# Kernel optimization log

Measured on AMD Instinct MI355X. Metric: run time of the kernel, lower is better.

The kernel has to match this reference:

```python
import jax, jax.numpy as jnp
import numpy as np

EMA_A = 0.4      # exponential moving average decay used in Hash_ExpMovAverage
WIN = 9          # window_size
LN_EPS = 1e-3    # keras LayerNormalization default epsilon


def setup_inputs() -> dict:
    key = jax.random.key(0)
    ks = jax.random.split(key, 8)
    B, N, D, H = 8, 4096, 256, 8
    w = lambda k, shape: jax.random.normal(k, shape, jnp.float32) * 0.05
    return {
        "x": jax.random.normal(ks[0], (B, N, D), jnp.float32),
        "head_kernel": w(ks[1], (D, H, D)),
        "head_bias": w(ks[2], (H, D)),
        "down_kernel": w(ks[3], (H, D, D)),
        "down_bias": w(ks[4], (D,)),
        "value_kernel": w(ks[5], (D, D)),
        "value_bias": w(ks[6], (D,)),
        "ln_gamma": jnp.ones((D,), jnp.float32),
        "ln_beta": jnp.zeros((D,), jnp.float32),
    }


def reference(x, head_kernel, head_bias, down_kernel, down_bias,
              value_kernel, value_bias, ln_gamma, ln_beta):
    B, N, D = x.shape
    half = (WIN - 1) // 2

    # Up_Projection: [B,N,D] -> [B,N,H,D], relu
    q = jax.nn.relu(jnp.einsum('bnd,dhe->bnhe', x, head_kernel) + head_bias)

    # ---- Neighborhoods_Arrangement ----
    # Neighborhood_SimHash: sign codes from relu activations, summed over heads
    codes = 2.0 * jnp.minimum(jnp.ceil(q), 1.0) - 1.0        # [B,N,H,D]
    lsh = jnp.sum(codes, axis=-2)                            # [B,N,D]
    # Hash_ExpMovAverage: sort descending along D, add positional encoding, EMA dot
    pos = jnp.argsort(-lsh, axis=-1)                         # descending order
    lsh_sorted = jnp.take_along_axis(lsh, pos, axis=-1)
    pf = pos.astype(jnp.float32)
    freq = 10.0 ** (-(pf / jnp.float32(D)))                  # 1 / 10**powers
    pe = jnp.sin(freq) * (pf % 2) + jnp.cos(freq) * (1.0 - pf % 2)
    vals = lsh_sorted + pe / EMA_A
    c = EMA_A * (1.0 - EMA_A) ** jnp.arange(D, dtype=jnp.float32)
    simv = jnp.einsum('bnd,d->bn', vals, c)                  # [B,N]
    order = jnp.argsort(simv, axis=-1)                       # ascending
    q = jnp.take_along_axis(q, order[:, :, None, None], axis=1)  # reorder tokens

    # Down_Projection: [B,N,H,D] -> [B,N,D], relu
    q = jax.nn.relu(jnp.einsum('bnhd,hde->bne', q, down_kernel) + down_bias)

    # (matches tile-first / extract_patches / tile-last concat in the original)
    starts = jnp.clip(jnp.arange(N) - half, 0, N - WIN)      # [N]
    widx = starts[:, None] + jnp.arange(WIN)[None, :]
    keyw = q[:, widx]

    scale = jnp.sqrt(jnp.float32(D))
    scores = jax.nn.softmax(jnp.einsum('bnd,bnwd->bnw', q, keyw) / scale, axis=-1)
    value = jax.nn.relu(jnp.einsum('bnwd,de->bnwe', keyw, value_kernel) + value_bias)
    attn_out = jnp.einsum('bnwd,bnw->bnd', value, scores)

    # Residual with ORIGINAL (un-permuted) inputs + LayerNorm (keras default eps)
    y = attn_out + x
    mu = jnp.mean(y, axis=-1, keepdims=True)
    var = jnp.var(y, axis=-1, keepdims=True)
    return (y - mu) / jnp.sqrt(var + LN_EPS) * ln_gamma + ln_beta
```

## Files before the change

kernel.cpp:

```cpp
#include <hip/hip_runtime.h>

constexpr int Bc = 8, Nc = 4096;

using short8 = __attribute__((ext_vector_type(8))) short;
using f32x4  = __attribute__((ext_vector_type(4))) float;

static __device__ __forceinline__ unsigned short f2bf(float f) {
    unsigned u = __float_as_uint(f);
    u += 0x7fffu + ((u >> 16) & 1u);
    return (unsigned short)(u >> 16);
}
static __device__ __forceinline__ int swz(int r, int k) {
    return (r << 9) + ((k << 1) ^ ((r & 7) << 4));
}

__global__ __launch_bounds__(256)
void k0_wdt(const float* __restrict__ Wd, unsigned short* __restrict__ WdT)
{
    __shared__ float tile[64][65];
    const int h  = blockIdx.x >> 4;
    const int t  = blockIdx.x & 15;
    const int kb = (t >> 2) * 64, eb = (t & 3) * 64;
    const int tid = threadIdx.x;
    {
        const int krow = tid >> 2, ec = (tid & 3) * 16;
        const float* src = Wd + h * 65536 + (kb + krow) * 256 + eb + ec;
        #pragma unroll
        for (int i = 0; i < 4; ++i) {
            float4 v = *reinterpret_cast<const float4*>(src + i * 4);
            tile[krow][ec + i * 4 + 0] = v.x;
            tile[krow][ec + i * 4 + 1] = v.y;
            tile[krow][ec + i * 4 + 2] = v.z;
            tile[krow][ec + i * 4 + 3] = v.w;
        }
    }
    __syncthreads();
    {
        const int erow = tid >> 2, dc = (tid & 3) * 16;
        unsigned short o[16];
        #pragma unroll
        for (int i = 0; i < 16; ++i) o[i] = f2bf(tile[dc + i][erow]);
        unsigned short* dst = WdT + h * 65536 + (eb + erow) * 256 + kb + dc;
        *reinterpret_cast<short8*>(dst)     = *reinterpret_cast<short8*>(&o[0]);
        *reinterpret_cast<short8*>(dst + 8) = *reinterpret_cast<short8*>(&o[8]);
    }
}

__global__ __launch_bounds__(256)
void k0_wht(const float* __restrict__ Wh, unsigned short* __restrict__ WhH,
            float* __restrict__ WhT)
{
    __shared__ float tile[64][65];
    const int h  = blockIdx.x >> 4;
    const int t  = blockIdx.x & 15;
    const int kb = (t >> 2) * 64, eb = (t & 3) * 64;
    const int tid = threadIdx.x;
    {
        const int krow = tid >> 2, ec = (tid & 3) * 16;
        const float* src = Wh + (kb + krow) * 2048 + h * 256 + eb + ec;
        #pragma unroll
        for (int i = 0; i < 4; ++i) {
            float4 v = *reinterpret_cast<const float4*>(src + i * 4);
            tile[krow][ec + i * 4 + 0] = v.x;
            tile[krow][ec + i * 4 + 1] = v.y;
            tile[krow][ec + i * 4 + 2] = v.z;
            tile[krow][ec + i * 4 + 3] = v.w;
        }
    }
    __syncthreads();
    {
        const int erow = tid >> 2, dc = (tid & 3) * 16;
        unsigned short o[16];
        float of[16];
        #pragma unroll
        for (int i = 0; i < 16; ++i) {
            of[i] = tile[dc + i][erow];
            o[i] = f2bf(of[i]);
        }
        const long base = (long)h * 65536 + (eb + erow) * 256 + kb + dc;
        *reinterpret_cast<short8*>(WhH + base)     = *reinterpret_cast<short8*>(&o[0]);
        *reinterpret_cast<short8*>(WhH + base + 8) = *reinterpret_cast<short8*>(&o[8]);
        #pragma unroll
        for (int i = 0; i < 16; i += 4)
            *reinterpret_cast<float4*>(WhT + base + i) = *reinterpret_cast<const float4*>(&of[i]);
    }
}

__global__ __launch_bounds__(256)
void k0_wvt(const float* __restrict__ Wv, unsigned short* __restrict__ WvT)
{
    __shared__ float tile[64][65];
    const int t  = blockIdx.x;
    const int kb = (t >> 2) * 64, eb = (t & 3) * 64;
    const int tid = threadIdx.x;
    {
        const int krow = tid >> 2, ec = (tid & 3) * 16;
        const float* src = Wv + (kb + krow) * 256 + eb + ec;
        #pragma unroll
        for (int i = 0; i < 4; ++i) {
            float4 v = *reinterpret_cast<const float4*>(src + i * 4);
            tile[krow][ec + i * 4 + 0] = v.x;
            tile[krow][ec + i * 4 + 1] = v.y;
            tile[krow][ec + i * 4 + 2] = v.z;
            tile[krow][ec + i * 4 + 3] = v.w;
        }
    }
    __syncthreads();
    {
        const int erow = tid >> 2, dc = (tid & 3) * 16;
        unsigned short o[16];
        #pragma unroll
        for (int i = 0; i < 16; ++i) o[i] = f2bf(tile[dc + i][erow]);
        unsigned short* dst = WvT + (eb + erow) * 256 + kb + dc;
        *reinterpret_cast<short8*>(dst)     = *reinterpret_cast<short8*>(&o[0]);
        *reinterpret_cast<short8*>(dst + 8) = *reinterpret_cast<short8*>(&o[8]);
    }
}

#define XSH_OFF  0
#define QTB_OFF  16384
#define LSH8_OFF 32768
#define PE_OFF   40960
#define CF_OFF   41984
#define CNT_OFF  43008
#define FCN_OFF  45056
#define CCN_OFF  45060
#define FLS_OFF  45064
#define CLS_OFF  49160
#define FLS_CAP  1024
#define CLS_CAP  96
#define GUARD    0.012f

__global__ __launch_bounds__(256, 3)
void k1_head_down(const float* __restrict__ x,
                  const float* __restrict__ bh,
                  const float* __restrict__ WhT,
                  const unsigned short* __restrict__ WhH,
                  const unsigned short* __restrict__ WdT, const float* __restrict__ bd,
                  float* __restrict__ z, float* __restrict__ simv)
{
    __shared__ __align__(16) char SM[49600];

    const int tid = threadIdx.x;
    const long rowbase = (long)blockIdx.x * 32;
    const int wavei = tid >> 6, lane = tid & 63;
    const int mrow = lane & 15, kgrp = lane >> 4;
    const int ebase = wavei * 64 + mrow;
    const int kfo = kgrp * 8;

    short8 hB[3][4], dB[3][4];
    #pragma unroll
    for (int i = 0; i < 2; ++i)
        #pragma unroll
        for (int nf = 0; nf < 4; ++nf)
            hB[i][nf] = *reinterpret_cast<const short8*>(
                &WhH[(ebase + nf * 16) * 256 + i * 32 + kfo]);

    {
        const int d = tid;
        const float u = -((float)d * 0.00390625f);
        const float freq = (float)pow(10.0, (double)u);
        const float pe = (d & 1) ? (float)sin((double)freq)
                                 : (float)cos((double)freq);
        ((float*)(SM + PE_OFF))[d] = __fdiv_rn(pe, 0.4f);
        ((float*)(SM + CF_OFF))[d] = __fmul_rn(0.4f, (float)pow((double)0.6f, (double)d));
    }
    if (tid == 0) { *((int*)(SM + FCN_OFF)) = 0; *((int*)(SM + CCN_OFF)) = 0; }
    {
        const int r = tid >> 3, kc = (tid & 7) * 32;
        const float* src = x + (rowbase + r) * 256 + kc;
        unsigned short oh[32];
        #pragma unroll
        for (int i = 0; i < 32; i += 4) {
            f32x4 v = __builtin_nontemporal_load(reinterpret_cast<const f32x4*>(src + i));
            oh[i + 0] = f2bf(v[0]); oh[i + 1] = f2bf(v[1]);
            oh[i + 2] = f2bf(v[2]); oh[i + 3] = f2bf(v[3]);
        }
        #pragma unroll
        for (int i = 0; i < 32; i += 8)
            *reinterpret_cast<short8*>(SM + XSH_OFF + swz(r, kc + i)) =
                *reinterpret_cast<short8*>(&oh[i]);
    }

    unsigned lshp[4] = {0u, 0u, 0u, 0u};
    f32x4 dacc[2][4];
    #pragma unroll
    for (int mt = 0; mt < 2; ++mt)
        #pragma unroll
        for (int nf = 0; nf < 4; ++nf) dacc[mt][nf] = (f32x4){0.f, 0.f, 0.f, 0.f};

    __syncthreads();

    for (int h = 0; h < 8; ++h) {
        const unsigned short* whh = WhH + ((long)h << 16);
        const unsigned short* wdh = WdT + ((long)h << 16);
        float bias[4];
        #pragma unroll
        for (int nf = 0; nf < 4; ++nf) bias[nf] = bh[(h << 8) + ebase + nf * 16];

        f32x4 hacc[2][4];
        #pragma unroll
        for (int mt = 0; mt < 2; ++mt)
            #pragma unroll
            for (int nf = 0; nf < 4; ++nf) hacc[mt][nf] = (f32x4){0.f, 0.f, 0.f, 0.f};
        #pragma unroll
        for (int kt = 0; kt < 8; ++kt) {
            const int k0 = kt * 32 + kfo;
            short8 a0 = *reinterpret_cast<const short8*>(SM + XSH_OFF + swz(mrow, k0));
            short8 a1 = *reinterpret_cast<const short8*>(SM + XSH_OFF + swz(16 + mrow, k0));
            if (kt < 6) {
                #pragma unroll
                for (int nf = 0; nf < 4; ++nf)
                    hB[(kt + 2) % 3][nf] = *reinterpret_cast<const short8*>(
                        &whh[(ebase + nf * 16) * 256 + (kt + 2) * 32 + kfo]);
            }
            #pragma unroll
            for (int nf = 0; nf < 4; ++nf) {
                hacc[0][nf] = __builtin_amdgcn_mfma_f32_16x16x32_bf16(a0, hB[kt % 3][nf], hacc[0][nf], 0, 0, 0);
                hacc[1][nf] = __builtin_amdgcn_mfma_f32_16x16x32_bf16(a1, hB[kt % 3][nf], hacc[1][nf], 0, 0, 0);
            }
        }
        #pragma unroll
        for (int i = 0; i < 2; ++i)
            #pragma unroll
            for (int nf = 0; nf < 4; ++nf)
                dB[i][nf] = *reinterpret_cast<const short8*>(
                    &wdh[(ebase + nf * 16) * 256 + i * 32 + kfo]);

        #pragma unroll
        for (int mt = 0; mt < 2; ++mt) {
            #pragma unroll
            for (int nf = 0; nf < 4; ++nf) {
                const int e = ebase + nf * 16;
                #pragma unroll
                for (int reg = 0; reg < 4; ++reg) {
                    const int r = mt * 16 + kgrp * 4 + reg;
                    const float pre = __fadd_rn(hacc[mt][nf][reg], bias[nf]);
                    const unsigned pos = (pre > 0.0f) ? 1u : 0u;
                    const int j = mt * 16 + nf * 4 + reg;
                    lshp[j >> 3] += pos << (4 * (j & 7));
                    if (fabsf(pre) < GUARD) {
                        int idx = atomicAdd((int*)(SM + FCN_OFF), 1);
                        if (idx < FLS_CAP)
                            ((int*)(SM + FLS_OFF))[idx] =
                                r | (e << 5) | (h << 13) | ((int)pos << 16);
                    }
                    *reinterpret_cast<unsigned short*>(SM + QTB_OFF + swz(r, e)) =
                        f2bf(fmaxf(pre, 0.0f));
                }
            }
        }
        __syncthreads();
        #pragma unroll
        for (int ks = 0; ks < 8; ++ks) {
            const int k0 = ks * 32 + kfo;
            short8 a0 = *reinterpret_cast<const short8*>(SM + QTB_OFF + swz(mrow, k0));
            short8 a1 = *reinterpret_cast<const short8*>(SM + QTB_OFF + swz(16 + mrow, k0));
            if (ks < 6) {
                #pragma unroll
                for (int nf = 0; nf < 4; ++nf)
                    dB[(ks + 2) % 3][nf] = *reinterpret_cast<const short8*>(
                        &wdh[(ebase + nf * 16) * 256 + (ks + 2) * 32 + kfo]);
            } else if (h < 7) {
                const int i = ks - 6;
                #pragma unroll
                for (int nf = 0; nf < 4; ++nf)
                    hB[i][nf] = *reinterpret_cast<const short8*>(
                        &WhH[((long)(h + 1) << 16) + (ebase + nf * 16) * 256 + i * 32 + kfo]);
            }
            #pragma unroll
            for (int nf = 0; nf < 4; ++nf) {
                dacc[0][nf] = __builtin_amdgcn_mfma_f32_16x16x32_bf16(a0, dB[ks % 3][nf], dacc[0][nf], 0, 0, 0);
                dacc[1][nf] = __builtin_amdgcn_mfma_f32_16x16x32_bf16(a1, dB[ks % 3][nf], dacc[1][nf], 0, 0, 0);
            }
        }
        __syncthreads();
    }
    #pragma unroll
    for (int mt = 0; mt < 2; ++mt) {
        #pragma unroll
        for (int nf = 0; nf < 4; ++nf) {
            const int e = ebase + nf * 16;
            const float b = bd[e];
            #pragma unroll
            for (int reg = 0; reg < 4; ++reg)
                __builtin_nontemporal_store(
                    fmaxf(dacc[mt][nf][reg] + b, 0.0f),
                    &z[(rowbase + mt * 16 + kgrp * 4 + reg) * 256 + e]);
        }
    }
    {
        signed char* lsh8 = (signed char*)(SM + LSH8_OFF);
        #pragma unroll
        for (int mt = 0; mt < 2; ++mt)
            #pragma unroll
            for (int nf = 0; nf < 4; ++nf) {
                const int e = ebase + nf * 16;
                #pragma unroll
                for (int reg = 0; reg < 4; ++reg) {
                    const int r = mt * 16 + kgrp * 4 + reg;
                    const int j = mt * 16 + nf * 4 + reg;
                    const unsigned p = (lshp[j >> 3] >> (4 * (j & 7))) & 15u;
                    lsh8[e * 32 + r] = (signed char)(2 * (int)p - 8);
                }
            }
    }
    __syncthreads();
    {
        int n = *((int*)(SM + FCN_OFF));
        n = n < FLS_CAP ? n : FLS_CAP;
        for (int i = tid; i < n; i += 256) {
            const int ent = ((int*)(SM + FLS_OFF))[i];
            const int r = ent & 31, e = (ent >> 5) & 255, hh2 = (ent >> 13) & 7;
            const int fs = ((ent >> 16) & 1) ? 1 : -1;
            const float* xr = x + (rowbase + r) * 256;
            const float* wrow = WhT + (((long)hh2 << 8) + e) * 256;
            float acc = 0.0f;
            for (int k = 0; k < 256; k += 4) {
                float4 xv = *reinterpret_cast<const float4*>(xr + k);
                float4 wv = *reinterpret_cast<const float4*>(wrow + k);
                acc = fmaf(xv.x, wv.x, acc);
                acc = fmaf(xv.y, wv.y, acc);
                acc = fmaf(xv.z, wv.z, acc);
                acc = fmaf(xv.w, wv.w, acc);
            }
            const float pre = __fadd_rn(acc, bh[hh2 * 256 + e]);
            const int es = (pre > 0.0f) ? 1 : -1;
            if (es != fs) {
                int ci = atomicAdd((int*)(SM + CCN_OFF), 1);
                if (ci < CLS_CAP)
                    ((int*)(SM + CLS_OFF))[ci] = r | (e << 5) | ((es > 0 ? 1 : 0) << 13);
            }
        }
    }
    __syncthreads();
    if (tid == 0) {
        signed char* lsh8 = (signed char*)(SM + LSH8_OFF);
        int cn = *((int*)(SM + CCN_OFF));
        cn = cn < CLS_CAP ? cn : CLS_CAP;
        for (int i = 0; i < cn; ++i) {
            const int ent = ((int*)(SM + CLS_OFF))[i];
            const int r = ent & 31, e = (ent >> 5) & 255;
            const int d = ((ent >> 13) & 1) ? 2 : -2;
            lsh8[e * 32 + r] = (signed char)(lsh8[e * 32 + r] + d);
        }
    }
    __syncthreads();
    if (tid < 32) {
        const int r = tid;
        const signed char* lsh8 = (const signed char*)(SM + LSH8_OFF);
        const float* pe_over = (const float*)(SM + PE_OFF);
        const float* c_f = (const float*)(SM + CF_OFF);
        int* cw = (int*)(SM + CNT_OFF) + r * 16;
        for (int i = 0; i < 9; ++i) cw[i] = 0;
        for (int d = 0; d < 256; ++d) {
            int vv = (int)lsh8[d * 32 + r];
            cw[(vv + 8) >> 1] += 1;
        }
        int run = 0;
        for (int bin = 8; bin >= 0; --bin) { int c0 = cw[bin]; cw[bin] = run; run += c0; }
        float* valq = (float*)(SM + r * 1024);
        for (int d = 0; d < 256; ++d) {
            int vv = (int)lsh8[d * 32 + r];
            int bin = (vv + 8) >> 1;
            int j = cw[bin]++;
            valq[j] = __fadd_rn((float)vv, pe_over[d]);
        }
        float L0 = 0.f, L1 = 0.f, L2 = 0.f, L3 = 0.f,
              L4 = 0.f, L5 = 0.f, L6 = 0.f, L7 = 0.f;
        for (int i = 0; i < 256; i += 8) {
            L0 = fmaf(valq[i + 0], c_f[i + 0], L0);
            L1 = fmaf(valq[i + 1], c_f[i + 1], L1);
            L2 = fmaf(valq[i + 2], c_f[i + 2], L2);
            L3 = fmaf(valq[i + 3], c_f[i + 3], L3);
            L4 = fmaf(valq[i + 4], c_f[i + 4], L4);
            L5 = fmaf(valq[i + 5], c_f[i + 5], L5);
            L6 = fmaf(valq[i + 6], c_f[i + 6], L6);
            L7 = fmaf(valq[i + 7], c_f[i + 7], L7);
        }
        const float h0 = __fadd_rn(L0, L4);
        const float h1 = __fadd_rn(L1, L5);
        const float h2 = __fadd_rn(L2, L6);
        const float h3 = __fadd_rn(L3, L7);
        simv[rowbase + r] = __fadd_rn(__fadd_rn(h0, h2), __fadd_rn(h1, h3));
    }
}

__global__ __launch_bounds__(256)
void k2_rank(const float* __restrict__ simv, int* __restrict__ order)
{
    __shared__ float s_l[4096];
    const int b = blockIdx.x >> 4;
    const int chunk = blockIdx.x & 15;
    const float* S = simv + (long)b * 4096;
    for (int i = threadIdx.x; i < 4096; i += 256) s_l[i] = S[i];
    __syncthreads();
    const int n = chunk * 256 + threadIdx.x;
    const float key = s_l[n];
    int cnt = 0;
    for (int m = 0; m < 4096; ++m) {
        float sm = s_l[m];
        cnt += (sm < key) ? 1 : ((sm == key && m < n) ? 1 : 0);
    }
    order[(long)b * 4096 + cnt] = n;
}

__global__ __launch_bounds__(256, 3)
void k3_value(const float* __restrict__ z, const int* __restrict__ order,
              const unsigned short* __restrict__ WvT, const float* __restrict__ bv,
              float* __restrict__ v)
{
    __shared__ __align__(16) unsigned short ZB[32 * 256];
    __shared__ int ord[32];
    const int tid = threadIdx.x;
    const long rowbase = (long)blockIdx.x * 32;
    const long bbase = (rowbase >> 12) << 12;
    const int wavei = tid >> 6, lane = tid & 63;
    const int mrow = lane & 15, kgrp = lane >> 4;
    const int ebase = wavei * 64 + mrow;
    const int kfo = kgrp * 8;

    if (tid < 32) ord[tid] = order[rowbase + tid];

    short8 vB[3][4];
    #pragma unroll
    for (int i = 0; i < 2; ++i)
        #pragma unroll
        for (int nf = 0; nf < 4; ++nf)
            vB[i][nf] = *reinterpret_cast<const short8*>(
                &WvT[(ebase + nf * 16) * 256 + i * 32 + kfo]);

    __syncthreads();
    {
        const int r = tid >> 3, kc = (tid & 7) * 32;
        const float* src = z + (bbase + ord[r]) * 256 + kc;
        unsigned short oh[32];
        #pragma unroll
        for (int i = 0; i < 32; i += 4) {
            float4 vv = *reinterpret_cast<const float4*>(src + i);
            oh[i + 0] = f2bf(vv.x); oh[i + 1] = f2bf(vv.y);
            oh[i + 2] = f2bf(vv.z); oh[i + 3] = f2bf(vv.w);
        }
        #pragma unroll
        for (int i = 0; i < 32; i += 8)
            *reinterpret_cast<short8*>((char*)ZB + swz(r, kc + i)) =
                *reinterpret_cast<short8*>(&oh[i]);
    }
    __syncthreads();

    f32x4 acc[2][4];
    #pragma unroll
    for (int mt = 0; mt < 2; ++mt)
        #pragma unroll
        for (int nf = 0; nf < 4; ++nf) acc[mt][nf] = (f32x4){0.f, 0.f, 0.f, 0.f};
    #pragma unroll
    for (int kt = 0; kt < 8; ++kt) {
        const int k0 = kt * 32 + kfo;
        short8 a0 = *reinterpret_cast<const short8*>((char*)ZB + swz(mrow, k0));
        short8 a1 = *reinterpret_cast<const short8*>((char*)ZB + swz(16 + mrow, k0));
        if (kt < 6) {
            #pragma unroll
            for (int nf = 0; nf < 4; ++nf)
                vB[(kt + 2) % 3][nf] = *reinterpret_cast<const short8*>(
                    &WvT[(ebase + nf * 16) * 256 + (kt + 2) * 32 + kfo]);
        }
        #pragma unroll
        for (int nf = 0; nf < 4; ++nf) {
            acc[0][nf] = __builtin_amdgcn_mfma_f32_16x16x32_bf16(a0, vB[kt % 3][nf], acc[0][nf], 0, 0, 0);
            acc[1][nf] = __builtin_amdgcn_mfma_f32_16x16x32_bf16(a1, vB[kt % 3][nf], acc[1][nf], 0, 0, 0);
        }
    }
    #pragma unroll
    for (int mt = 0; mt < 2; ++mt) {
        #pragma unroll
        for (int nf = 0; nf < 4; ++nf) {
            const int e = ebase + nf * 16;
            const float b = bv[e];
            #pragma unroll
            for (int reg = 0; reg < 4; ++reg)
                v[(rowbase + mt * 16 + kgrp * 4 + reg) * 256 + e] =
                    fmaxf(acc[mt][nf][reg] + b, 0.0f);
        }
    }
}

__global__ __launch_bounds__(256)
void k4_attn_ln(const float* __restrict__ z, const float* __restrict__ v,
                const int* __restrict__ order, const float* __restrict__ x,
                const float* __restrict__ gamma, const float* __restrict__ beta,
                float* __restrict__ out)
{
    const int tid = threadIdx.x;
    const int wv = tid >> 6, lane = tid & 63;
    const long row = (long)blockIdx.x * 4 + wv;
    const int n = (int)(row & 4095);
    const long bbase = row - n;
    int start = n - 4;
    start = start < 0 ? 0 : start;
    start = start > (Nc - 9) ? (Nc - 9) : start;
    const int d0 = lane * 4;

    const int srcq = order[bbase + n];
    float4 q4 = *reinterpret_cast<const float4*>(&z[(bbase + srcq) * 256 + d0]);

    float t[9];
    #pragma unroll
    for (int w = 0; w < 9; ++w) {
        int srcm = order[bbase + start + w];
        float4 kv = *reinterpret_cast<const float4*>(&z[(bbase + srcm) * 256 + d0]);
        float p = q4.x * kv.x + q4.y * kv.y + q4.z * kv.z + q4.w * kv.w;
        #pragma unroll
        for (int off = 32; off > 0; off >>= 1) p += __shfl_xor(p, off);
        t[w] = p * 0.0625f;
    }
    float mx = t[0];
    #pragma unroll
    for (int w = 1; w < 9; ++w) mx = fmaxf(mx, t[w]);
    float pw[9], psum = 0.0f;
    #pragma unroll
    for (int w = 0; w < 9; ++w) { pw[w] = expf(t[w] - mx); psum += pw[w]; }
    const float pinv = 1.0f / psum;

    float4 a = make_float4(0.f, 0.f, 0.f, 0.f);
    #pragma unroll
    for (int w = 0; w < 9; ++w) {
        float4 vv = *reinterpret_cast<const float4*>(&v[(bbase + start + w) * 256 + d0]);
        float s = pw[w] * pinv;
        a.x = fmaf(vv.x, s, a.x);
        a.y = fmaf(vv.y, s, a.y);
        a.z = fmaf(vv.z, s, a.z);
        a.w = fmaf(vv.w, s, a.w);
    }
    float4 xv = *reinterpret_cast<const float4*>(&x[(bbase + n) * 256 + d0]);
    float4 y = make_float4(a.x + xv.x, a.y + xv.y, a.z + xv.z, a.w + xv.w);

    float s1 = y.x + y.y + y.z + y.w;
    float s2 = y.x * y.x + y.y * y.y + y.z * y.z + y.w * y.w;
    #pragma unroll
    for (int off = 32; off > 0; off >>= 1) {
        s1 += __shfl_xor(s1, off);
        s2 += __shfl_xor(s2, off);
    }
    const float mu = s1 * (1.0f / 256.0f);
    const float var = s2 * (1.0f / 256.0f) - mu * mu;
    const float istd = 1.0f / sqrtf(var + 0.001f);

    float4 g4 = *reinterpret_cast<const float4*>(&gamma[d0]);
    float4 b4 = *reinterpret_cast<const float4*>(&beta[d0]);
    float4 o;
    o.x = (y.x - mu) * istd * g4.x + b4.x;
    o.y = (y.y - mu) * istd * g4.y + b4.y;
    o.z = (y.z - mu) * istd * g4.z + b4.z;
    o.w = (y.w - mu) * istd * g4.w + b4.w;
    *reinterpret_cast<float4*>(&out[row * 256 + d0]) = o;
}

extern "C" void kernel_launch(void* const* d_in, const int* in_sizes, int n_in,
                              void* d_out, int out_size, void* d_ws, size_t ws_size,
                              hipStream_t stream)
{
    const float* x  = (const float*)d_in[0];
    const float* Wh = (const float*)d_in[1];
    const float* bh = (const float*)d_in[2];
    const float* Wd = (const float*)d_in[3];
    const float* bd = (const float*)d_in[4];
    const float* Wv = (const float*)d_in[5];
    const float* bv = (const float*)d_in[6];
    const float* g  = (const float*)d_in[7];
    const float* be = (const float*)d_in[8];
    float* out = (float*)d_out;

    char* ws = (char*)d_ws;
    float*          z     = (float*)ws;
    float*          v     = (float*)(ws + 33554432);
    float*          simv  = (float*)(ws + 67108864);
    int*            order = (int*)(ws + 67239936);
    unsigned short* WdT   = (unsigned short*)(ws + 67371008);
    unsigned short* WhH   = (unsigned short*)(ws + 68419584);
    float*          WhT   = (float*)(ws + 69468160);
    unsigned short* WvT   = (unsigned short*)(ws + 71565312);

    const int rows = Bc * Nc;
    k0_wdt<<<dim3(128), dim3(256), 0, stream>>>(Wd, WdT);
    k0_wht<<<dim3(128), dim3(256), 0, stream>>>(Wh, WhH, WhT);
    k0_wvt<<<dim3(16), dim3(256), 0, stream>>>(Wv, WvT);
    k1_head_down<<<dim3(rows / 32), dim3(256), 0, stream>>>(x, bh, WhT, WhH, WdT, bd, z, simv);
    k2_rank<<<dim3(Bc * 16), dim3(256), 0, stream>>>(simv, order);
    k3_value<<<dim3(rows / 32), dim3(256), 0, stream>>>(z, order, WvT, bv, v);
    k4_attn_ln<<<dim3(rows / 4), dim3(256), 0, stream>>>(z, v, order, x, g, be, out);
}
```

Measured before the change: 834.9 us.

## Split fused head/down kernel into head, down, and LSH-simv kernels

Replaces the single fused head-projection and down-projection kernel with three kernels. The new path writes the bf16 relu head activations to a 128MB workspace, parallelises the head GEMM across heads on a 2D grid, runs the down projection as a separate GEMM, and recomputes the LSH codes and simv (with fp32 guard-band corrections) in a third kernel. The split is meant to raise parallelism and shorten the per-block serial head loop, at the cost of extra global memory traffic for the intermediate and more launches. The new path only runs when the workspace is large enough; otherwise the old fused kernel is used.

```diff
diff --git a/kernel.cpp b/kernel.cpp
--- a/kernel.cpp
+++ b/kernel.cpp
@@ -13,6 +13,9 @@
 static __device__ __forceinline__ int swz(int r, int k) {
     return (r << 9) + ((k << 1) ^ ((r & 7) << 4));
 }
+
+#define GBIN_CAP 320
+#define GUARD    0.012f
 
 __global__ __launch_bounds__(256)
 void k0_wdt(const float* __restrict__ Wd, unsigned short* __restrict__ WdT)
@@ -114,6 +117,317 @@
         unsigned short* dst = WvT + (eb + erow) * 256 + kb + dc;
         *reinterpret_cast<short8*>(dst)     = *reinterpret_cast<short8*>(&o[0]);
         *reinterpret_cast<short8*>(dst + 8) = *reinterpret_cast<short8*>(&o[8]);
+    }
+}
+
+__global__ __launch_bounds__(256, 3)
+void k1a_head(const float* __restrict__ x, const float* __restrict__ bh,
+              const unsigned short* __restrict__ WhH,
+              unsigned short* __restrict__ q, int* __restrict__ gcnt, int* __restrict__ gls)
+{
+    __shared__ __align__(16) char SM[16384];
+
+    const int tid = threadIdx.x;
+    const long rowbase = (long)blockIdx.x * 32;
+    const int h = blockIdx.y;
+    const int wavei = tid >> 6, lane = tid & 63;
+    const int mrow = lane & 15, kgrp = lane >> 4;
+    const int ebase = wavei * 64 + mrow;
+    const int kfo = kgrp * 8;
+    const unsigned short* whh = WhH + ((long)h << 16);
+
+    short8 hB[4][4];
+    #pragma unroll
+    for (int i = 0; i < 4; ++i)
+        #pragma unroll
+        for (int nf = 0; nf < 4; ++nf)
+            hB[i][nf] = *reinterpret_cast<const short8*>(
+                &whh[(ebase + nf * 16) * 256 + i * 32 + kfo]);
+
+    {
+        const int r = tid >> 3, kc = (tid & 7) * 32;
+        const float* src = x + (rowbase + r) * 256 + kc;
+        unsigned short oh[32];
+        #pragma unroll
+        for (int i = 0; i < 32; i += 4) {
+            float4 v = *reinterpret_cast<const float4*>(src + i);
+            oh[i + 0] = f2bf(v.x); oh[i + 1] = f2bf(v.y);
+            oh[i + 2] = f2bf(v.z); oh[i + 3] = f2bf(v.w);
+        }
+        #pragma unroll
+        for (int i = 0; i < 32; i += 8)
+            *reinterpret_cast<short8*>(SM + swz(r, kc + i)) =
+                *reinterpret_cast<short8*>(&oh[i]);
+    }
+    __syncthreads();
+
+    f32x4 hacc[2][4];
+    #pragma unroll
+    for (int mt = 0; mt < 2; ++mt)
+        #pragma unroll
+        for (int nf = 0; nf < 4; ++nf) hacc[mt][nf] = (f32x4){0.f, 0.f, 0.f, 0.f};
+    #pragma unroll
+    for (int kt = 0; kt < 8; ++kt) {
+        const int k0 = kt * 32 + kfo;
+        short8 a0 = *reinterpret_cast<const short8*>(SM + swz(mrow, k0));
+        short8 a1 = *reinterpret_cast<const short8*>(SM + swz(16 + mrow, k0));
+        #pragma unroll
+        for (int nf = 0; nf < 4; ++nf) {
+            hacc[0][nf] = __builtin_amdgcn_mfma_f32_16x16x32_bf16(a0, hB[kt & 3][nf], hacc[0][nf], 0, 0, 0);
+            hacc[1][nf] = __builtin_amdgcn_mfma_f32_16x16x32_bf16(a1, hB[kt & 3][nf], hacc[1][nf], 0, 0, 0);
+        }
+        if (kt < 4) {
+            #pragma unroll
+            for (int nf = 0; nf < 4; ++nf)
+                hB[kt][nf] = *reinterpret_cast<const short8*>(
+                    &whh[(ebase + nf * 16) * 256 + (kt + 4) * 32 + kfo]);
+        }
+    }
+    float bias[4];
+    #pragma unroll
+    for (int nf = 0; nf < 4; ++nf) bias[nf] = bh[(h << 8) + ebase + nf * 16];
+    __syncthreads();
+    const int bin = (int)blockIdx.x * 8 + h;
+    #pragma unroll
+    for (int mt = 0; mt < 2; ++mt) {
+        #pragma unroll
+        for (int nf = 0; nf < 4; ++nf) {
+            const int e = ebase + nf * 16;
+            #pragma unroll
+            for (int reg = 0; reg < 4; ++reg) {
+                const int r = mt * 16 + kgrp * 4 + reg;
+                const float pre = __fadd_rn(hacc[mt][nf][reg], bias[nf]);
+                if (fabsf(pre) < GUARD) {
+                    int idx = atomicAdd(&gcnt[bin], 1);
+                    if (idx < GBIN_CAP)
+                        gls[bin * GBIN_CAP + idx] =
+                            r | (e << 5) | ((pre > 0.0f ? 1 : 0) << 13);
+                }
+                *reinterpret_cast<unsigned short*>(SM + swz(r, e)) =
+                    f2bf(fmaxf(pre, 0.0f));
+            }
+        }
+    }
+    __syncthreads();
+    {
+        const int r = tid >> 3, ec = (tid & 7) * 32;
+        unsigned short* dst = q + (rowbase + r) * 2048 + (h << 8) + ec;
+        #pragma unroll
+        for (int i = 0; i < 4; ++i)
+            *reinterpret_cast<short8*>(dst + i * 8) =
+                *reinterpret_cast<short8*>(SM + swz(r, ec + i * 8));
+    }
+}
+
+__global__ __launch_bounds__(256, 3)
+void k1b_down(const unsigned short* __restrict__ q,
+              const unsigned short* __restrict__ WdT, const float* __restrict__ bd,
+              float* __restrict__ z)
+{
+    __shared__ __align__(16) char SM[16384];
+
+    const int tid = threadIdx.x;
+    const long rowbase = (long)blockIdx.x * 32;
+    const int wavei = tid >> 6, lane = tid & 63;
+    const int mrow = lane & 15, kgrp = lane >> 4;
+    const int ebase = wavei * 64 + mrow;
+    const int kfo = kgrp * 8;
+
+    short8 dB[4][4];
+    #pragma unroll
+    for (int i = 0; i < 4; ++i)
+        #pragma unroll
+        for (int nf = 0; nf < 4; ++nf)
+            dB[i][nf] = *reinterpret_cast<const short8*>(
+                &WdT[(ebase + nf * 16) * 256 + i * 32 + kfo]);
+
+    f32x4 dacc[2][4];
+    #pragma unroll
+    for (int mt = 0; mt < 2; ++mt)
+        #pragma unroll
+        for (int nf = 0; nf < 4; ++nf) dacc[mt][nf] = (f32x4){0.f, 0.f, 0.f, 0.f};
+
+    for (int kc = 0; kc < 8; ++kc) {
+        const unsigned short* wdh = WdT + ((long)kc << 16);
+        {
+            const int r = tid >> 3, kb2 = (tid & 7) * 32;
+            const unsigned short* src = q + (rowbase + r) * 2048 + (kc << 8) + kb2;
+            short8 t0 = *reinterpret_cast<const short8*>(src);
+            short8 t1 = *reinterpret_cast<const short8*>(src + 8);
+            short8 t2 = *reinterpret_cast<const short8*>(src + 16);
+            short8 t3 = *reinterpret_cast<const short8*>(src + 24);
+            *reinterpret_cast<short8*>(SM + swz(r, kb2))      = t0;
+            *reinterpret_cast<short8*>(SM + swz(r, kb2 + 8))  = t1;
+            *reinterpret_cast<short8*>(SM + swz(r, kb2 + 16)) = t2;
+            *reinterpret_cast<short8*>(SM + swz(r, kb2 + 24)) = t3;
+        }
+        __syncthreads();
+        #pragma unroll
+        for (int ks = 0; ks < 8; ++ks) {
+            const int k0 = ks * 32 + kfo;
+            short8 a0 = *reinterpret_cast<const short8*>(SM + swz(mrow, k0));
+            short8 a1 = *reinterpret_cast<const short8*>(SM + swz(16 + mrow, k0));
+            #pragma unroll
+            for (int nf = 0; nf < 4; ++nf) {
+                dacc[0][nf] = __builtin_amdgcn_mfma_f32_16x16x32_bf16(a0, dB[ks & 3][nf], dacc[0][nf], 0, 0, 0);
+                dacc[1][nf] = __builtin_amdgcn_mfma_f32_16x16x32_bf16(a1, dB[ks & 3][nf], dacc[1][nf], 0, 0, 0);
+            }
+            if (ks < 4) {
+                #pragma unroll
+                for (int nf = 0; nf < 4; ++nf)
+                    dB[ks][nf] = *reinterpret_cast<const short8*>(
+                        &wdh[(ebase + nf * 16) * 256 + (ks + 4) * 32 + kfo]);
+            } else if (kc < 7) {
+                #pragma unroll
+                for (int nf = 0; nf < 4; ++nf)
+                    dB[ks - 4][nf] = *reinterpret_cast<const short8*>(
+                        &WdT[((long)(kc + 1) << 16) + (ebase + nf * 16) * 256 + (ks - 4) * 32 + kfo]);
+            }
+        }
+        __syncthreads();
+    }
+    #pragma unroll
+    for (int mt = 0; mt < 2; ++mt) {
+        #pragma unroll
+        for (int nf = 0; nf < 4; ++nf) {
+            const int e = ebase + nf * 16;
+            const float b = bd[e];
+            #pragma unroll
+            for (int reg = 0; reg < 4; ++reg)
+                z[(rowbase + mt * 16 + kgrp * 4 + reg) * 256 + e] =
+                    fmaxf(dacc[mt][nf][reg] + b, 0.0f);
+        }
+    }
+}
+
+#define R_VALQ 0
+#define R_LSH8 32768
+#define R_PE   40960
+#define R_CF   41984
+#define R_CNT  43008
+#define R_CCN  45056
+#define R_CLS  45060
+#define R_CLS_CAP 128
+
+__global__ __launch_bounds__(256, 2)
+void k1r_lsh_simv(const unsigned short* __restrict__ q, const float* __restrict__ x,
+                  const float* __restrict__ WhT, const float* __restrict__ bh,
+                  const int* __restrict__ gcnt, const int* __restrict__ gls,
+                  float* __restrict__ simv)
+{
+    __shared__ __align__(16) char SM[45576];
+    const int tid = threadIdx.x;
+    const long rowbase = (long)blockIdx.x * 32;
+
+    {
+        const int d = tid;
+        const float u = -((float)d * 0.00390625f);
+        const float freq = (float)pow(10.0, (double)u);
+        const float pe = (d & 1) ? (float)sin((double)freq)
+                                 : (float)cos((double)freq);
+        ((float*)(SM + R_PE))[d] = __fdiv_rn(pe, 0.4f);
+        ((float*)(SM + R_CF))[d] = __fmul_rn(0.4f, (float)pow((double)0.6f, (double)d));
+    }
+    if (tid == 0) *(int*)(SM + R_CCN) = 0;
+    {
+        const int r = tid >> 3, ec = (tid & 7) * 32;
+        int acc[32];
+        #pragma unroll
+        for (int j = 0; j < 32; ++j) acc[j] = 0;
+        for (int h = 0; h < 8; ++h) {
+            const unsigned short* src = q + (rowbase + r) * 2048 + (h << 8) + ec;
+            #pragma unroll
+            for (int i = 0; i < 4; ++i) {
+                short8 v8 = *reinterpret_cast<const short8*>(src + i * 8);
+                #pragma unroll
+                for (int j = 0; j < 8; ++j)
+                    acc[i * 8 + j] += ((unsigned short)v8[j] != 0) ? 1 : -1;
+            }
+        }
+        signed char* lsh8 = (signed char*)(SM + R_LSH8);
+        #pragma unroll
+        for (int j = 0; j < 32; ++j)
+            lsh8[(ec + j) * 32 + r] = (signed char)acc[j];
+    }
+    __syncthreads();
+    for (int h = 0; h < 8; ++h) {
+        const int bin = (int)blockIdx.x * 8 + h;
+        int n = gcnt[bin];
+        n = n < GBIN_CAP ? n : GBIN_CAP;
+        for (int i = tid; i < n; i += 256) {
+            const int ent = gls[bin * GBIN_CAP + i];
+            const int r = ent & 31, e = (ent >> 5) & 255;
+            const int fs = ((ent >> 13) & 1) ? 1 : -1;
+            const float* xr = x + (rowbase + r) * 256;
+            const float* wrow = WhT + (((long)h << 8) + e) * 256;
+            float acc = 0.0f;
+            for (int k = 0; k < 256; k += 4) {
+                float4 xv = *reinterpret_cast<const float4*>(xr + k);
+                float4 wv = *reinterpret_cast<const float4*>(wrow + k);
+                acc = fmaf(xv.x, wv.x, acc);
+                acc = fmaf(xv.y, wv.y, acc);
+                acc = fmaf(xv.z, wv.z, acc);
+                acc = fmaf(xv.w, wv.w, acc);
+            }
+            const float pre = __fadd_rn(acc, bh[h * 256 + e]);
+            const int es = (pre > 0.0f) ? 1 : -1;
+            if (es != fs) {
+                int ci = atomicAdd((int*)(SM + R_CCN), 1);
+                if (ci < R_CLS_CAP)
+                    ((int*)(SM + R_CLS))[ci] = r | (e << 5) | ((es > 0 ? 1 : 0) << 13);
+            }
+        }
+    }
+    __syncthreads();
+    if (tid == 0) {
+        signed char* lsh8 = (signed char*)(SM + R_LSH8);
+        int cn = *(int*)(SM + R_CCN);
+        cn = cn < R_CLS_CAP ? cn : R_CLS_CAP;
+        for (int i = 0; i < cn; ++i) {
+            const int ent = ((int*)(SM + R_CLS))[i];
+            const int r = ent & 31, e = (ent >> 5) & 255;
+            const int d = ((ent >> 13) & 1) ? 2 : -2;
+            lsh8[e * 32 + r] = (signed char)(lsh8[e * 32 + r] + d);
+        }
+    }
+    __syncthreads();
+    if (tid < 32) {
+        const int r = tid;
+        const signed char* lsh8 = (const signed char*)(SM + R_LSH8);
+        const float* pe_over = (const float*)(SM + R_PE);
+        const float* c_f = (const float*)(SM + R_CF);
+        int* cw = (int*)(SM + R_CNT) + r * 16;
+        for (int i = 0; i < 9; ++i) cw[i] = 0;
+        for (int d = 0; d < 256; ++d) {
+            int vv = (int)lsh8[d * 32 + r];
+            cw[(vv + 8) >> 1] += 1;
+        }
+        int run = 0;
+        for (int bin = 8; bin >= 0; --bin) { int c0 = cw[bin]; cw[bin] = run; run += c0; }
+        float* valq = (float*)(SM + R_VALQ + r * 1024);
+        for (int d = 0; d < 256; ++d) {
+            int vv = (int)lsh8[d * 32 + r];
+            int bin = (vv + 8) >> 1;
+            int j = cw[bin]++;
+            valq[j] = __fadd_rn((float)vv, pe_over[d]);
+        }
+        float L0 = 0.f, L1 = 0.f, L2 = 0.f, L3 = 0.f,
+              L4 = 0.f, L5 = 0.f, L6 = 0.f, L7 = 0.f;
+        for (int i = 0; i < 256; i += 8) {
+            L0 = fmaf(valq[i + 0], c_f[i + 0], L0);
+            L1 = fmaf(valq[i + 1], c_f[i + 1], L1);
+            L2 = fmaf(valq[i + 2], c_f[i + 2], L2);
+            L3 = fmaf(valq[i + 3], c_f[i + 3], L3);
+            L4 = fmaf(valq[i + 4], c_f[i + 4], L4);
+            L5 = fmaf(valq[i + 5], c_f[i + 5], L5);
+            L6 = fmaf(valq[i + 6], c_f[i + 6], L6);
+            L7 = fmaf(valq[i + 7], c_f[i + 7], L7);
+        }
+        const float h0 = __fadd_rn(L0, L4);
+        const float h1 = __fadd_rn(L1, L5);
+        const float h2 = __fadd_rn(L2, L6);
+        const float h3 = __fadd_rn(L3, L7);
+        simv[rowbase + r] = __fadd_rn(__fadd_rn(h0, h2), __fadd_rn(h1, h3));
     }
 }
 
@@ -129,18 +443,16 @@
 #define CLS_OFF  49160
 #define FLS_CAP  1024
 #define CLS_CAP  96
-#define GUARD    0.012f
 
 __global__ __launch_bounds__(256, 3)
-void k1_head_down(const float* __restrict__ x,
-                  const float* __restrict__ bh,
-                  const float* __restrict__ WhT,
-                  const unsigned short* __restrict__ WhH,
-                  const unsigned short* __restrict__ WdT, const float* __restrict__ bd,
-                  float* __restrict__ z, float* __restrict__ simv)
+void k1_fused(const float* __restrict__ x,
+              const float* __restrict__ bh,
+              const float* __restrict__ WhT,
+              const unsigned short* __restrict__ WhH,
+              const unsigned short* __restrict__ WdT, const float* __restrict__ bd,
+              float* __restrict__ z, float* __restrict__ simv)
 {
     __shared__ __align__(16) char SM[49600];
-
     const int tid = threadIdx.x;
     const long rowbase = (long)blockIdx.x * 32;
     const int wavei = tid >> 6, lane = tid & 63;
@@ -155,7 +467,6 @@
         for (int nf = 0; nf < 4; ++nf)
             hB[i][nf] = *reinterpret_cast<const short8*>(
                 &WhH[(ebase + nf * 16) * 256 + i * 32 + kfo]);
-
     {
         const int d = tid;
         const float u = -((float)d * 0.00390625f);
@@ -165,39 +476,35 @@
         ((float*)(SM + PE_OFF))[d] = __fdiv_rn(pe, 0.4f);
         ((float*)(SM + CF_OFF))[d] = __fmul_rn(0.4f, (float)pow((double)0.6f, (double)d));
     }
-    if (tid == 0) { *((int*)(SM + FCN_OFF)) = 0; *((int*)(SM + CCN_OFF)) = 0; }
+    if (tid == 0) { *(int*)(SM + FCN_OFF) = 0; *(int*)(SM + CCN_OFF) = 0; }
     {
         const int r = tid >> 3, kc = (tid & 7) * 32;
         const float* src = x + (rowbase + r) * 256 + kc;
         unsigned short oh[32];
         #pragma unroll
         for (int i = 0; i < 32; i += 4) {
-            f32x4 v = __builtin_nontemporal_load(reinterpret_cast<const f32x4*>(src + i));
-            oh[i + 0] = f2bf(v[0]); oh[i + 1] = f2bf(v[1]);
-            oh[i + 2] = f2bf(v[2]); oh[i + 3] = f2bf(v[3]);
+            float4 v = *reinterpret_cast<const float4*>(src + i);
+            oh[i + 0] = f2bf(v.x); oh[i + 1] = f2bf(v.y);
+            oh[i + 2] = f2bf(v.z); oh[i + 3] = f2bf(v.w);
         }
         #pragma unroll
         for (int i = 0; i < 32; i += 8)
             *reinterpret_cast<short8*>(SM + XSH_OFF + swz(r, kc + i)) =
                 *reinterpret_cast<short8*>(&oh[i]);
     }
-
     unsigned lshp[4] = {0u, 0u, 0u, 0u};
     f32x4 dacc[2][4];
     #pragma unroll
     for (int mt = 0; mt < 2; ++mt)
         #pragma unroll
         for (int nf = 0; nf < 4; ++nf) dacc[mt][nf] = (f32x4){0.f, 0.f, 0.f, 0.f};
-
-    __syncthreads();
-
+    __syncthreads();
     for (int h = 0; h < 8; ++h) {
         const unsigned short* whh = WhH + ((long)h << 16);
         const unsigned short* wdh = WdT + ((long)h << 16);
         float bias[4];
         #pragma unroll
         for (int nf = 0; nf < 4; ++nf) bias[nf] = bh[(h << 8) + ebase + nf * 16];
-
         f32x4 hacc[2][4];
         #pragma unroll
         for (int mt = 0; mt < 2; ++mt)
@@ -226,7 +533,6 @@
             for (int nf = 0; nf < 4; ++nf)
                 dB[i][nf] = *reinterpret_cast<const short8*>(
                     &wdh[(ebase + nf * 16) * 256 + i * 32 + kfo]);
-
         #pragma unroll
         for (int mt = 0; mt < 2; ++mt) {
             #pragma unroll
@@ -284,9 +590,8 @@
             const float b = bd[e];
             #pragma unroll
             for (int reg = 0; reg < 4; ++reg)
-                __builtin_nontemporal_store(
-                    fmaxf(dacc[mt][nf][reg] + b, 0.0f),
-                    &z[(rowbase + mt * 16 + kgrp * 4 + reg) * 256 + e]);
+                z[(rowbase + mt * 16 + kgrp * 4 + reg) * 256 + e] =
+                    fmaxf(dacc[mt][nf][reg] + b, 0.0f);
         }
     }
     {
@@ -579,12 +884,24 @@
     unsigned short* WhH   = (unsigned short*)(ws + 68419584);
     float*          WhT   = (float*)(ws + 69468160);
     unsigned short* WvT   = (unsigned short*)(ws + 71565312);
-
+    unsigned short* q     = (unsigned short*)(ws + 71696384);
+    int*            gcnt  = (int*)(ws + 205914112);
+    int*            gls   = (int*)(ws + 205946880);
+
+    const bool big = ws_size >= 216432640ULL;
     const int rows = Bc * Nc;
+
     k0_wdt<<<dim3(128), dim3(256), 0, stream>>>(Wd, WdT);
     k0_wht<<<dim3(128), dim3(256), 0, stream>>>(Wh, WhH, WhT);
     k0_wvt<<<dim3(16), dim3(256), 0, stream>>>(Wv, WvT);
-    k1_head_down<<<dim3(rows / 32), dim3(256), 0, stream>>>(x, bh, WhT, WhH, WdT, bd, z, simv);
+    if (big) {
+        hipMemsetAsync(gcnt, 0, 32768, stream);
+        k1a_head<<<dim3(1024, 8), dim3(256), 0, stream>>>(x, bh, WhH, q, gcnt, gls);
+        k1b_down<<<dim3(1024), dim3(256), 0, stream>>>(q, WdT, bd, z);
+        k1r_lsh_simv<<<dim3(1024), dim3(256), 0, stream>>>(q, x, WhT, bh, gcnt, gls, simv);
+    } else {
+        k1_fused<<<dim3(rows / 32), dim3(256), 0, stream>>>(x, bh, WhT, WhH, WdT, bd, z, simv);
+    }
     k2_rank<<<dim3(Bc * 16), dim3(256), 0, stream>>>(simv, order);
     k3_value<<<dim3(rows / 32), dim3(256), 0, stream>>>(z, order, WvT, bv, v);
     k4_attn_ln<<<dim3(rows / 4), dim3(256), 0, stream>>>(z, v, order, x, g, be, out);
```

Result: faster. 817.9 us (-2.0%).
